# Kernel tuning notes

Measured on AMD Instinct MI355X. Metric: run time of the kernel, lower is better.

The kernel has to match this reference:

```python
import jax, jax.numpy as jnp
import numpy as np

N, S, E, H = 2, 2048, 1024, 16
D = E // H  # head_dim = 64


def setup_inputs() -> dict:
    key = jax.random.key(0)
    k1, k2, k3 = jax.random.split(key, 3)
    x = jax.random.normal(k1, (N, S, E), dtype=jnp.float32)
    # Xavier-uniform-scaled weights (torch Linear layout: [out_features, in_features])
    lim_qkv = (6.0 / (E + 3 * E)) ** 0.5
    qkv_w = jax.random.uniform(k2, (3 * E, E), dtype=jnp.float32, minval=-lim_qkv, maxval=lim_qkv)
    lim_o = (6.0 / (E + E)) ** 0.5
    o_w = jax.random.uniform(k3, (E, E), dtype=jnp.float32, minval=-lim_o, maxval=lim_o)
    # causal look-ahead mask: positions where mask == 0 are excluded
    attn_mask = jnp.tril(jnp.ones((S, S), dtype=jnp.int32))
    return {"x": x, "attn_mask": attn_mask, "qkv_w": qkv_w, "o_w": o_w}


def reference(x, attn_mask, qkv_w, o_w):
    n, s, e = x.shape
    qkv = x @ qkv_w.T                              # (N, S, 3E)
    q, k, v = jnp.split(qkv, 3, axis=-1)
    # (N, S, E) -> (N, H, S, D)
    def to_heads(t):
        return t.reshape(n, s, H, D).transpose(0, 2, 1, 3)
    q, k, v = to_heads(q), to_heads(k), to_heads(v)
    scale = 1.0 / jnp.sqrt(jnp.asarray(D, dtype=x.dtype))
    logits = jnp.einsum('bhqd,bhkd->bhqk', q, k) * scale   # (N, H, S, S)
    mask = attn_mask.reshape(1, 1, s, s)                    # expand_mask: 2D -> (1,1,S,S)
    logits = jnp.where(mask == 0, -jnp.inf, logits)
    attn_weights = jax.nn.softmax(logits, axis=-1)
    values = jnp.einsum('bhqk,bhkd->bhqd', attn_weights, v)  # (N, H, S, D)
    values = values.transpose(0, 2, 1, 3).reshape(n, s, e)
    o = values @ o_w.T
    return o
```

## Files before the change

kernel.cpp:

```cpp
#include <hip/hip_runtime.h>
#include <math.h>

typedef unsigned short u16;
typedef unsigned int uint;
typedef __attribute__((ext_vector_type(8))) short bf16x8;
typedef __attribute__((ext_vector_type(8))) _Float16 half8;
typedef __attribute__((ext_vector_type(4))) float floatx4;

__device__ __forceinline__ u16 f2bf(float f) {
  union { float f; uint u; } c; c.f = f;
  return (u16)((c.u + 0x7FFFu + ((c.u >> 16) & 1u)) >> 16);
}
__device__ __forceinline__ float bf2f(u16 h) {
  union { uint u; float f; } c; c.u = ((uint)h) << 16;
  return c.f;
}
__device__ __forceinline__ u16 h2u(_Float16 h) {
  union { _Float16 h; u16 u; } c; c.h = h;
  return c.u;
}

#if __has_builtin(__builtin_amdgcn_exp2f)
#define EX2 __builtin_amdgcn_exp2f
#else
#define EX2 exp2f
#endif

__device__ __forceinline__ void gl_lds16(const u16* g, u16* l) {
  __builtin_amdgcn_global_load_lds(
      (const __attribute__((address_space(1))) uint*)g,
      (__attribute__((address_space(3))) uint*)l, 16, 0, 0);
}

__device__ __forceinline__ void store_c(u16* p, float v) { *p = f2bf(v); }
__device__ __forceinline__ void store_c(float* p, float v) { *p = v; }

#define ROR16(x, n)                                                        \
  __builtin_bit_cast(float, __builtin_amdgcn_update_dpp(                   \
      __builtin_bit_cast(int, (x)), __builtin_bit_cast(int, (x)),          \
      0x120 + (n), 0xF, 0xF, false))
__device__ __forceinline__ float rsum16(float x) {
  x += ROR16(x, 8); x += ROR16(x, 4); x += ROR16(x, 2); x += ROR16(x, 1);
  return x;
}

__global__ __launch_bounds__(256) void cvt_all(const float* __restrict__ x,
                                               const float* __restrict__ qw,
                                               const float* __restrict__ ow,
                                               u16* __restrict__ xb,
                                               u16* __restrict__ wb,
                                               u16* __restrict__ ob) {
  int bx = blockIdx.x;
  const float* src; u16* dst; int off;
  if (bx < 2048) { src = x; dst = xb; off = bx; }
  else if (bx < 3584) { src = qw; dst = wb; off = bx - 2048; }
  else { src = ow; dst = ob; off = bx - 3584; }
  int i = (off * 256 + threadIdx.x) * 8;
  float4 a = *(const float4*)(src + i);
  float4 b = *(const float4*)(src + i + 4);
  bf16x8 r;
  r[0] = (short)f2bf(a.x); r[1] = (short)f2bf(a.y);
  r[2] = (short)f2bf(a.z); r[3] = (short)f2bf(a.w);
  r[4] = (short)f2bf(b.x); r[5] = (short)f2bf(b.y);
  r[6] = (short)f2bf(b.z); r[7] = (short)f2bf(b.w);
  *(bf16x8*)(dst + i) = r;
}

__global__ __launch_bounds__(256) void vtrans(const u16* __restrict__ qkv,
                                              u16* __restrict__ vt) {
  constexpr int S = 2048, E = 1024, TE = 3072;
  __shared__ u16 tile[64 * 72];
  const int t = threadIdx.x;
  const int kv0 = blockIdx.x * 64;
  const int bh = blockIdx.y, b = bh >> 4, h = bh & 15;
  const u16* src = qkv + (size_t)b * S * TE + 2 * E + h * 64;
#pragma unroll
  for (int i = 0; i < 2; ++i) {
    int c = t + i * 256;
    int kv = c >> 3, d0 = (c & 7) * 8;
    *(bf16x8*)&tile[kv * 72 + d0] = *(const bf16x8*)&src[(size_t)(kv0 + kv) * TE + d0];
  }
  __syncthreads();
  u16* dst = vt + (size_t)bh * 64 * S + kv0;
#pragma unroll
  for (int i = 0; i < 2; ++i) {
    int c = t + i * 256;
    int d = c >> 3, k0 = (c & 7) * 8;
    bf16x8 r;
#pragma unroll
    for (int j = 0; j < 8; ++j)
      r[j] = (short)h2u((_Float16)bf2f(tile[(k0 + j) * 72 + d]));
    *(bf16x8*)&dst[(size_t)d * S + k0] = r;
  }
}

template <typename TC>
__global__ __launch_bounds__(256) void gemm_bt(const u16* __restrict__ A,
                                               const u16* __restrict__ B,
                                               TC* __restrict__ C,
                                               int K, int N) {
  __shared__ __align__(16) u16 lds_a[128 * 64];
  __shared__ __align__(16) u16 lds_b[128 * 64];
  const int t = threadIdx.x;
  const int w = t >> 6, lane = t & 63, quad = lane >> 4, lr = lane & 15;
  const int wr = w >> 1, wc = w & 1;
  const int m0 = blockIdx.y * 128, n0 = blockIdx.x * 128;

  const int srow = lane >> 3;
  const int scol = ((lane & 7) ^ srow) * 8;
  const u16* Ab = A + (size_t)(m0 + w * 32 + srow) * K + scol;
  const u16* Bb = B + (size_t)(n0 + w * 32 + srow) * K + scol;
  u16* la = lds_a + (w * 32) * 64;
  u16* lb = lds_b + (w * 32) * 64;

  floatx4 acc[4][4];
#pragma unroll
  for (int i = 0; i < 4; ++i)
#pragma unroll
    for (int j = 0; j < 4; ++j) acc[i][j] = {0.f, 0.f, 0.f, 0.f};

  for (int k0 = 0; k0 < K; k0 += 64) {
#pragma unroll
    for (int j = 0; j < 4; ++j) {
      gl_lds16(Ab + (size_t)(j * 8) * K + k0, la + j * 8 * 64);
      gl_lds16(Bb + (size_t)(j * 8) * K + k0, lb + j * 8 * 64);
    }
    __syncthreads();
#pragma unroll
    for (int kk = 0; kk < 2; ++kk) {
      bf16x8 af[4], bfr[4];
#pragma unroll
      for (int mi = 0; mi < 4; ++mi)
        af[mi] = *(const bf16x8*)&lds_a[(wr * 64 + mi * 16 + lr) * 64 +
                                        (((kk * 4 + quad) ^ (lr & 7)) * 8)];
#pragma unroll
      for (int ni = 0; ni < 4; ++ni)
        bfr[ni] = *(const bf16x8*)&lds_b[(wc * 64 + ni * 16 + lr) * 64 +
                                         (((kk * 4 + quad) ^ (lr & 7)) * 8)];
#pragma unroll
      for (int mi = 0; mi < 4; ++mi)
#pragma unroll
        for (int ni = 0; ni < 4; ++ni)
          acc[mi][ni] = __builtin_amdgcn_mfma_f32_16x16x32_bf16(
              af[mi], bfr[ni], acc[mi][ni], 0, 0, 0);
    }
    __syncthreads();
  }
#pragma unroll
  for (int mi = 0; mi < 4; ++mi)
#pragma unroll
    for (int r = 0; r < 4; ++r) {
      int m = m0 + wr * 64 + mi * 16 + quad * 4 + r;
#pragma unroll
      for (int ni = 0; ni < 4; ++ni) {
        int n = n0 + wc * 64 + ni * 16 + lr;
        store_c(&C[(size_t)m * N + n], acc[mi][ni][r]);
      }
    }
}

template <typename TC>
__global__ __launch_bounds__(256) void gemm_bt64(const u16* __restrict__ A,
                                                 const u16* __restrict__ B,
                                                 TC* __restrict__ C,
                                                 int K, int N) {
  __shared__ __align__(16) u16 lds_a[64 * 64];
  __shared__ __align__(16) u16 lds_b[128 * 64];
  const int t = threadIdx.x;
  const int w = t >> 6, lane = t & 63, quad = lane >> 4, lr = lane & 15;
  const int m0 = blockIdx.y * 64, n0 = blockIdx.x * 128;

  const int srow = lane >> 3;
  const int scol = ((lane & 7) ^ srow) * 8;
  const u16* Ab = A + (size_t)(m0 + srow) * K + scol;
  const u16* Bb = B + (size_t)(n0 + srow) * K + scol;

  floatx4 acc[4][2];
#pragma unroll
  for (int i = 0; i < 4; ++i)
#pragma unroll
    for (int j = 0; j < 2; ++j) acc[i][j] = {0.f, 0.f, 0.f, 0.f};

  for (int k0 = 0; k0 < K; k0 += 64) {
#pragma unroll
    for (int i = 0; i < 2; ++i)
      gl_lds16(Ab + (size_t)((w * 2 + i) * 8) * K + k0, &lds_a[(w * 2 + i) * 8 * 64]);
#pragma unroll
    for (int i = 0; i < 4; ++i)
      gl_lds16(Bb + (size_t)((w * 4 + i) * 8) * K + k0, &lds_b[(w * 4 + i) * 8 * 64]);
    __syncthreads();
#pragma unroll
    for (int kk = 0; kk < 2; ++kk) {
      bf16x8 af[4], bfr[2];
#pragma unroll
      for (int mi = 0; mi < 4; ++mi)
        af[mi] = *(const bf16x8*)&lds_a[(mi * 16 + lr) * 64 +
                                        (((kk * 4 + quad) ^ (lr & 7)) * 8)];
#pragma unroll
      for (int ni = 0; ni < 2; ++ni)
        bfr[ni] = *(const bf16x8*)&lds_b[(w * 32 + ni * 16 + lr) * 64 +
                                         (((kk * 4 + quad) ^ (lr & 7)) * 8)];
#pragma unroll
      for (int mi = 0; mi < 4; ++mi)
#pragma unroll
        for (int ni = 0; ni < 2; ++ni)
          acc[mi][ni] = __builtin_amdgcn_mfma_f32_16x16x32_bf16(
              af[mi], bfr[ni], acc[mi][ni], 0, 0, 0);
    }
    __syncthreads();
  }
#pragma unroll
  for (int mi = 0; mi < 4; ++mi)
#pragma unroll
    for (int r = 0; r < 4; ++r) {
      int m = m0 + mi * 16 + quad * 4 + r;
#pragma unroll
      for (int ni = 0; ni < 2; ++ni) {
        int n = n0 + w * 32 + ni * 16 + lr;
        store_c(&C[(size_t)m * N + n], acc[mi][ni][r]);
      }
    }
}

__global__ __launch_bounds__(512, 2) void attn_fwd(const u16* __restrict__ qkv,
                                                   const u16* __restrict__ vt,
                                                   u16* __restrict__ out) {
  constexpr int S = 2048, E = 1024, TE = 3072;
  constexpr float NEG = -1e30f;
  __shared__ __align__(16) u16 lds_k[2][128 * 64];
  __shared__ __align__(16) u16 lds_vt[2][64 * 128];
  __shared__ __align__(16) u16 lds_p[2][4][16 * 128];
  const int t = threadIdx.x;
  const int wv = t >> 6;
  const int u = wv >> 2;
  const int w = wv & 3;
  const int lane = t & 63, quad = lane >> 4, lr = lane & 15;
  const int bx = (int)blockIdx.x;
  const int h = bx & 15, qt = bx >> 4;
  const int b = u;
  const int bh = b * 16 + h;
  const size_t base = (size_t)b * S * TE;
  const u16* kbase = qkv + base + E + h * 64;
  const u16* vtb = vt + (size_t)bh * 64 * S;

  const int s8 = lane >> 3;
  const int kcol = ((lane & 7) ^ s8) * 8;
  const int vrow = lane >> 4;
  u16* const pb = &lds_p[u][w][0];
  u16* const lk = &lds_k[u][0];
  u16* const lv = &lds_vt[u][0];

  const int q0 = qt * 128;
  const int nkt = qt + 1;

  const float QS = 0.125f * 1.44269504f;
  bf16x8 qf[2][2];
#pragma unroll
  for (int rg = 0; rg < 2; ++rg)
#pragma unroll
    for (int kk = 0; kk < 2; ++kk) {
      bf16x8 q = *(const bf16x8*)&qkv[base +
          (size_t)(q0 + w * 32 + rg * 16 + lr) * TE + h * 64 + kk * 32 + quad * 8];
#pragma unroll
      for (int jj = 0; jj < 8; ++jj) q[jj] = (short)f2bf(bf2f((u16)q[jj]) * QS);
      qf[rg][kk] = q;
    }

  float lst[2][4];
  floatx4 oacc[2][4];
#pragma unroll
  for (int rg = 0; rg < 2; ++rg)
#pragma unroll
    for (int r = 0; r < 4; ++r) { lst[rg][r] = 0.f; }
#pragma unroll
  for (int rg = 0; rg < 2; ++rg)
#pragma unroll
    for (int di = 0; di < 4; ++di) oacc[rg][di] = {0.f, 0.f, 0.f, 0.f};

#pragma unroll
  for (int i = 0; i < 4; ++i) {
    int p0 = w * 8 + i * 32;
    int kv = ((p0 & 15) + s8) * 8 + (p0 >> 4);
    gl_lds16(kbase + (size_t)kv * TE + kcol, &lk[p0 * 64]);
  }
#pragma unroll
  for (int i = 0; i < 4; ++i) {
    int d0 = w * 4 + i * 16;
    int d = d0 + vrow;
    int cbg = ((lane & 15) ^ (d & 15)) * 8;
    gl_lds16(vtb + (size_t)d * S + cbg, &lv[d0 * 128]);
  }

  for (int kt = 0; kt < nkt; ++kt) {
    __syncthreads();

    floatx4 st[2][8];
#pragma unroll
    for (int rg = 0; rg < 2; ++rg)
#pragma unroll
      for (int ni = 0; ni < 8; ++ni) st[rg][ni] = {-4.f, -4.f, -4.f, -4.f};
#pragma unroll
    for (int kk = 0; kk < 2; ++kk) {
      bf16x8 kb[8];
#pragma unroll
      for (int ni = 0; ni < 8; ++ni)
        kb[ni] = *(const bf16x8*)&lk[(ni * 16 + lr) * 64 +
                                     (((kk * 4 + quad) ^ (lr & 7)) * 8)];
#pragma unroll
      for (int rg = 0; rg < 2; ++rg)
#pragma unroll
        for (int ni = 0; ni < 8; ++ni)
          st[rg][ni] = __builtin_amdgcn_mfma_f32_16x16x32_bf16(
              qf[rg][kk], kb[ni], st[rg][ni], 0, 0, 0);
    }

    half8 vb[4][4];
#pragma unroll
    for (int kk = 0; kk < 4; ++kk)
#pragma unroll
      for (int di = 0; di < 4; ++di)
        vb[kk][di] = *(const half8*)&lv[(di * 16 + lr) * 128 +
                                        (((kk * 4 + quad) ^ lr) << 3)];

    __syncthreads();

    if (kt + 1 < nkt) {
#pragma unroll
      for (int i = 0; i < 4; ++i) {
        int p0 = w * 8 + i * 32;
        int kv = 128 * (kt + 1) + ((p0 & 15) + s8) * 8 + (p0 >> 4);
        gl_lds16(kbase + (size_t)kv * TE + kcol, &lk[p0 * 64]);
      }
#pragma unroll
      for (int i = 0; i < 4; ++i) {
        int d0 = w * 4 + i * 16;
        int d = d0 + vrow;
        int cbg = ((lane & 15) ^ (d & 15)) * 8;
        gl_lds16(vtb + (size_t)d * S + 128 * (kt + 1) + cbg, &lv[d0 * 128]);
      }
    }

    const bool diag = (kt == nkt - 1);
#pragma unroll
    for (int rg = 0; rg < 2; ++rg) {
#pragma unroll
      for (int r = 0; r < 4; ++r) {
        const int rw = quad * 4 + r;
        const int rloc = w * 32 + rg * 16 + rw;
        if (diag) {
#pragma unroll
          for (int ni = 0; ni < 8; ++ni)
            if (lr * 8 + ni > rloc) st[rg][ni][r] = NEG;
        }
        float pv[8];
#pragma unroll
        for (int ni = 0; ni < 8; ++ni) pv[ni] = EX2(st[rg][ni][r]);
        lst[rg][r] += ((pv[0] + pv[1]) + (pv[2] + pv[3])) +
                      ((pv[4] + pv[5]) + (pv[6] + pv[7]));
        half8 p8;
#pragma unroll
        for (int ni = 0; ni < 8; ++ni) p8[ni] = (_Float16)pv[ni];
        *(half8*)&pb[rw * 128 + (((lr + rw) & 15) << 3)] = p8;
      }
#pragma unroll
      for (int kk = 0; kk < 4; ++kk) {
        half8 pf = *(const half8*)&pb[lr * 128 +
                                      ((((kk * 4 + quad) + lr) & 15) << 3)];
#pragma unroll
        for (int di = 0; di < 4; ++di)
          oacc[rg][di] = __builtin_amdgcn_mfma_f32_16x16x32_f16(
              pf, vb[kk][di], oacc[rg][di], 0, 0, 0);
      }
    }
  }

#pragma unroll
  for (int rg = 0; rg < 2; ++rg)
#pragma unroll
    for (int r = 0; r < 4; ++r) {
      int sg = q0 + w * 32 + rg * 16 + quad * 4 + r;
      float inv_l = 1.f / rsum16(lst[rg][r]);
#pragma unroll
      for (int di = 0; di < 4; ++di)
        out[((size_t)(b * S + sg)) * E + h * 64 + di * 16 + lr] =
            f2bf(oacc[rg][di][r] * inv_l);
    }
}

extern "C" void kernel_launch(void* const* d_in, const int* in_sizes, int n_in,
                              void* d_out, int out_size, void* d_ws, size_t ws_size,
                              hipStream_t stream) {
  constexpr int NB = 2, S = 2048, E = 1024;
  constexpr int M = NB * S;
  const float* x = (const float*)d_in[0];
  const float* qkv_w = (const float*)d_in[2];
  const float* o_w = (const float*)d_in[3];
  float* out = (float*)d_out;

  u16* qkv = (u16*)d_ws;
  u16* vt = qkv + (size_t)M * 3 * E;
  u16* xb = vt + (size_t)32 * 64 * S;
  u16* attn_o = xb;
  u16* wb = xb + (size_t)M * E;
  u16* ob = wb + (size_t)3 * E * E;

  cvt_all<<<4096, 256, 0, stream>>>(x, qkv_w, o_w, xb, wb, ob);
  gemm_bt<u16><<<dim3(3 * E / 128, M / 128), 256, 0, stream>>>(xb, wb, qkv, E, 3 * E);
  vtrans<<<dim3(S / 64, NB * 16), 256, 0, stream>>>(qkv, vt);
  attn_fwd<<<256, 512, 0, stream>>>(qkv, vt, attn_o);
  gemm_bt64<float><<<dim3(E / 128, M / 64), 256, 0, stream>>>(attn_o, ob, out, E, E);
}
```

Measured before the change: 188.9 us.

## Balance causal attention work by pairing query tiles with split-KV partials

Each attention block used to own one query tile, so causal masking made blocks range from 1 to 16 KV iterations. Now each block gets a fixed 8 or 9 iterations. Blocks split the long tile 15-pr across two blocks, and one of them also processes the short tile pr. Unnormalized partial outputs and row sums for the split tiles go to a float workspace, and a new combine kernel sums and normalizes them into bf16. This shortens the critical path of the attention kernel, at the cost of an extra launch and extra global-memory traffic for the fp32 partials.

```diff
diff --git a/kernel.cpp b/kernel.cpp
--- a/kernel.cpp
+++ b/kernel.cpp
@@ -224,7 +224,9 @@
 
 __global__ __launch_bounds__(512, 2) void attn_fwd(const u16* __restrict__ qkv,
                                                    const u16* __restrict__ vt,
-                                                   u16* __restrict__ out) {
+                                                   u16* __restrict__ out,
+                                                   float* __restrict__ opart,
+                                                   float* __restrict__ lpart) {
   constexpr int S = 2048, E = 1024, TE = 3072;
   constexpr float NEG = -1e30f;
   __shared__ __align__(16) u16 lds_k[2][128 * 64];
@@ -236,9 +238,11 @@
   const int w = wv & 3;
   const int lane = t & 63, quad = lane >> 4, lr = lane & 15;
   const int bx = (int)blockIdx.x;
-  const int h = bx & 15, qt = bx >> 4;
+  const int h = bx & 15, pr = (bx >> 4) & 7, hB = bx >> 7;
+  const int qtH = 15 - pr;
   const int b = u;
   const int bh = b * 16 + h;
+  const int pid = (b * 16 + h) * 8 + pr;
   const size_t base = (size_t)b * S * TE;
   const u16* kbase = qkv + base + E + h * 64;
   const u16* vtb = vt + (size_t)bh * 64 * S;
@@ -250,48 +254,78 @@
   u16* const lk = &lds_k[u][0];
   u16* const lv = &lds_vt[u][0];
 
-  const int q0 = qt * 128;
-  const int nkt = qt + 1;
+  const int n0 = hB ? (8 - pr) : 8;
+  const int niter = hB ? 9 : 8;
 
   const float QS = 0.125f * 1.44269504f;
   bf16x8 qf[2][2];
-#pragma unroll
-  for (int rg = 0; rg < 2; ++rg)
-#pragma unroll
-    for (int kk = 0; kk < 2; ++kk) {
-      bf16x8 q = *(const bf16x8*)&qkv[base +
-          (size_t)(q0 + w * 32 + rg * 16 + lr) * TE + h * 64 + kk * 32 + quad * 8];
-#pragma unroll
-      for (int jj = 0; jj < 8; ++jj) q[jj] = (short)f2bf(bf2f((u16)q[jj]) * QS);
-      qf[rg][kk] = q;
-    }
-
   float lst[2][4];
   floatx4 oacc[2][4];
-#pragma unroll
-  for (int rg = 0; rg < 2; ++rg)
-#pragma unroll
-    for (int r = 0; r < 4; ++r) { lst[rg][r] = 0.f; }
-#pragma unroll
-  for (int rg = 0; rg < 2; ++rg)
-#pragma unroll
-    for (int di = 0; di < 4; ++di) oacc[rg][di] = {0.f, 0.f, 0.f, 0.f};
-
-#pragma unroll
-  for (int i = 0; i < 4; ++i) {
-    int p0 = w * 8 + i * 32;
-    int kv = ((p0 & 15) + s8) * 8 + (p0 >> 4);
-    gl_lds16(kbase + (size_t)kv * TE + kcol, &lk[p0 * 64]);
-  }
-#pragma unroll
-  for (int i = 0; i < 4; ++i) {
-    int d0 = w * 4 + i * 16;
-    int d = d0 + vrow;
-    int cbg = ((lane & 15) ^ (d & 15)) * 8;
-    gl_lds16(vtb + (size_t)d * S + cbg, &lv[d0 * 128]);
-  }
-
-  for (int kt = 0; kt < nkt; ++kt) {
+
+  auto load_q = [&](int qt) {
+#pragma unroll
+    for (int rg = 0; rg < 2; ++rg)
+#pragma unroll
+      for (int kk = 0; kk < 2; ++kk) {
+        bf16x8 q = *(const bf16x8*)&qkv[base +
+            (size_t)(qt * 128 + w * 32 + rg * 16 + lr) * TE + h * 64 + kk * 32 + quad * 8];
+#pragma unroll
+        for (int jj = 0; jj < 8; ++jj) q[jj] = (short)f2bf(bf2f((u16)q[jj]) * QS);
+        qf[rg][kk] = q;
+      }
+  };
+  auto reset_acc = [&]() {
+#pragma unroll
+    for (int rg = 0; rg < 2; ++rg) {
+#pragma unroll
+      for (int r = 0; r < 4; ++r) lst[rg][r] = 0.f;
+#pragma unroll
+      for (int di = 0; di < 4; ++di) oacc[rg][di] = {0.f, 0.f, 0.f, 0.f};
+    }
+  };
+  auto emit_partial = [&](int slot) {
+    float* op = opart + ((size_t)slot * 256 + pid) * (128 * 64);
+    float* lp = lpart + ((size_t)slot * 256 + pid) * 128;
+#pragma unroll
+    for (int rg = 0; rg < 2; ++rg)
+#pragma unroll
+      for (int r = 0; r < 4; ++r) {
+        int row = w * 32 + rg * 16 + quad * 4 + r;
+        float lt = rsum16(lst[rg][r]);
+        if (lr == 0) lp[row] = lt;
+#pragma unroll
+        for (int di = 0; di < 4; ++di)
+          op[row * 64 + di * 16 + lr] = oacc[rg][di][r];
+      }
+  };
+  auto kv_of = [&](int it) -> int {
+    if (!hB) return it;
+    return (it < n0) ? (8 + it) : (it - n0);
+  };
+
+  load_q(qtH);
+  reset_acc();
+
+  {
+    int nb = kv_of(0) * 128;
+#pragma unroll
+    for (int i = 0; i < 4; ++i) {
+      int p0 = w * 8 + i * 32;
+      int kv = nb + ((p0 & 15) + s8) * 8 + (p0 >> 4);
+      gl_lds16(kbase + (size_t)kv * TE + kcol, &lk[p0 * 64]);
+    }
+#pragma unroll
+    for (int i = 0; i < 4; ++i) {
+      int d0 = w * 4 + i * 16;
+      int d = d0 + vrow;
+      int cbg = ((lane & 15) ^ (d & 15)) * 8;
+      gl_lds16(vtb + (size_t)d * S + nb + cbg, &lv[d0 * 128]);
+    }
+  }
+
+  for (int it = 0; it < niter; ++it) {
+    const int kt = kv_of(it);
+    const int qcur = (hB && it >= n0) ? pr : qtH;
     __syncthreads();
 
     floatx4 st[2][8];
@@ -324,11 +358,12 @@
 
     __syncthreads();
 
-    if (kt + 1 < nkt) {
+    if (it + 1 < niter) {
+      int nb = kv_of(it + 1) * 128;
 #pragma unroll
       for (int i = 0; i < 4; ++i) {
         int p0 = w * 8 + i * 32;
-        int kv = 128 * (kt + 1) + ((p0 & 15) + s8) * 8 + (p0 >> 4);
+        int kv = nb + ((p0 & 15) + s8) * 8 + (p0 >> 4);
         gl_lds16(kbase + (size_t)kv * TE + kcol, &lk[p0 * 64]);
       }
 #pragma unroll
@@ -336,11 +371,11 @@
         int d0 = w * 4 + i * 16;
         int d = d0 + vrow;
         int cbg = ((lane & 15) ^ (d & 15)) * 8;
-        gl_lds16(vtb + (size_t)d * S + 128 * (kt + 1) + cbg, &lv[d0 * 128]);
-      }
-    }
-
-    const bool diag = (kt == nkt - 1);
+        gl_lds16(vtb + (size_t)d * S + nb + cbg, &lv[d0 * 128]);
+      }
+    }
+
+    const bool diag = (kt == qcur);
 #pragma unroll
     for (int rg = 0; rg < 2; ++rg) {
 #pragma unroll
@@ -372,19 +407,60 @@
               pf, vb[kk][di], oacc[rg][di], 0, 0, 0);
       }
     }
-  }
-
-#pragma unroll
-  for (int rg = 0; rg < 2; ++rg)
-#pragma unroll
-    for (int r = 0; r < 4; ++r) {
-      int sg = q0 + w * 32 + rg * 16 + quad * 4 + r;
-      float inv_l = 1.f / rsum16(lst[rg][r]);
-#pragma unroll
-      for (int di = 0; di < 4; ++di)
-        out[((size_t)(b * S + sg)) * E + h * 64 + di * 16 + lr] =
-            f2bf(oacc[rg][di][r] * inv_l);
-    }
+
+    if (hB && it == n0 - 1) {
+      emit_partial(1);
+      reset_acc();
+      load_q(pr);
+    }
+  }
+
+  if (!hB) {
+    emit_partial(0);
+  } else {
+#pragma unroll
+    for (int rg = 0; rg < 2; ++rg)
+#pragma unroll
+      for (int r = 0; r < 4; ++r) {
+        int sg = pr * 128 + w * 32 + rg * 16 + quad * 4 + r;
+        float inv_l = 1.f / rsum16(lst[rg][r]);
+#pragma unroll
+        for (int di = 0; di < 4; ++di)
+          out[((size_t)(b * S + sg)) * E + h * 64 + di * 16 + lr] =
+              f2bf(oacc[rg][di][r] * inv_l);
+      }
+  }
+}
+
+__global__ __launch_bounds__(256) void attn_combine(const float* __restrict__ opart,
+                                                    const float* __restrict__ lpart,
+                                                    u16* __restrict__ out) {
+  constexpr int S = 2048, E = 1024;
+  const int p = (int)blockIdx.x;
+  const int pr = p & 7, bh = p >> 3, h = bh & 15, b = bh >> 4;
+  const int q0 = (15 - pr) * 128;
+  const int t = threadIdx.x;
+  const int row = t >> 1, c0 = (t & 1) * 32;
+  const float* o0 = opart + (size_t)p * (128 * 64) + row * 64 + c0;
+  const float* o1 = o0 + (size_t)256 * 128 * 64;
+  float l = lpart[p * 128 + row] + lpart[256 * 128 + p * 128 + row];
+  float inv = 1.f / l;
+  u16* dst = out + ((size_t)(b * S + q0 + row)) * E + h * 64 + c0;
+#pragma unroll
+  for (int i = 0; i < 4; ++i) {
+    float4 a0 = ((const float4*)o0)[2 * i], a1 = ((const float4*)o0)[2 * i + 1];
+    float4 b0 = ((const float4*)o1)[2 * i], b1 = ((const float4*)o1)[2 * i + 1];
+    bf16x8 r;
+    r[0] = (short)f2bf((a0.x + b0.x) * inv);
+    r[1] = (short)f2bf((a0.y + b0.y) * inv);
+    r[2] = (short)f2bf((a0.z + b0.z) * inv);
+    r[3] = (short)f2bf((a0.w + b0.w) * inv);
+    r[4] = (short)f2bf((a1.x + b1.x) * inv);
+    r[5] = (short)f2bf((a1.y + b1.y) * inv);
+    r[6] = (short)f2bf((a1.z + b1.z) * inv);
+    r[7] = (short)f2bf((a1.w + b1.w) * inv);
+    ((bf16x8*)dst)[i] = r;
+  }
 }
 
 extern "C" void kernel_launch(void* const* d_in, const int* in_sizes, int n_in,
@@ -403,10 +479,13 @@
   u16* attn_o = xb;
   u16* wb = xb + (size_t)M * E;
   u16* ob = wb + (size_t)3 * E * E;
+  float* opart = (float*)(ob + (size_t)E * E);
+  float* lpart = opart + (size_t)2 * 256 * 128 * 64;
 
   cvt_all<<<4096, 256, 0, stream>>>(x, qkv_w, o_w, xb, wb, ob);
   gemm_bt<u16><<<dim3(3 * E / 128, M / 128), 256, 0, stream>>>(xb, wb, qkv, E, 3 * E);
   vtrans<<<dim3(S / 64, NB * 16), 256, 0, stream>>>(qkv, vt);
-  attn_fwd<<<256, 512, 0, stream>>>(qkv, vt, attn_o);
+  attn_fwd<<<256, 512, 0, stream>>>(qkv, vt, attn_o, opart, lpart);
+  attn_combine<<<256, 256, 0, stream>>>(opart, lpart, attn_o);
   gemm_bt64<float><<<dim3(E / 128, M / 64), 256, 0, stream>>>(attn_o, ob, out, E, E);
 }
```

New measurement: 199.7 us. 1.06x slower.
